# Performance work log

Measured on AMD Instinct MI355X. Metric: run time of the kernel, lower is better.

Reference implementation:

```python
import jax, jax.numpy as jnp
import numpy as np


def setup_inputs() -> dict:
    key = jax.random.key(0)
    k1, k2, k3 = jax.random.split(key, 3)
    N, D, B = 2000000, 128, 4096
    x = jax.random.normal(k1, (N, D), dtype=jnp.float32)
    batch = jnp.sort(jax.random.randint(k2, (N,), 0, B, dtype=jnp.int64))
    alpha = jax.random.normal(k3, (1,), dtype=jnp.float32)
    return {"x": x, "batch": batch, "alpha": alpha, "num_segments": B}


def reference(x, batch, alpha, num_segments):
    # Gating scalar in (0, 1)
    a = jax.nn.sigmoid(alpha)  # shape (1,), broadcasts
    # Segment mean: sum / count (count clamped to avoid div-by-zero on empty segments)
    seg_sum = jax.ops.segment_sum(x, batch, num_segments=num_segments)  # [B, D]
    counts = jax.ops.segment_sum(jnp.ones((x.shape[0],), dtype=x.dtype), batch,
                                 num_segments=num_segments)  # [B]
    mean = seg_sum / jnp.maximum(counts, 1.0)[:, None]  # [B, D]
    # Segment max; empty segments get -inf -> replace with 0 to match scatter-max fill
    mx = jax.ops.segment_max(x, batch, num_segments=num_segments)  # [B, D]
    mx = jnp.where(jnp.isfinite(mx), mx, 0.0)
    return a * mean + (1.0 - a) * mx
```

## Files before the change

### kernel.cpp

```cpp
#include <hip/hip_runtime.h>
#include <math.h>
#include <float.h>


__global__ void detect_kernel(const int* __restrict__ words, int N, int* __restrict__ meta) {
    meta[0] = (words[(size_t)N - 1] != 0) ? 1 : 2;
}

__global__ void starts_kernel(const int* __restrict__ words, int N, int B,
                              int* __restrict__ start, const int* __restrict__ meta) {
    int i = blockIdx.x * blockDim.x + threadIdx.x;
    if (i >= N) return;
    const int stride = meta[0];
    int cur = words[(size_t)i * stride];
    if (i == 0) {
        for (int b = 0; b <= cur; ++b) start[b] = 0;
    } else {
        int prev = words[(size_t)(i - 1) * stride];
        if (prev != cur) {
            for (int b = prev + 1; b <= cur; ++b) start[b] = i;
        }
    }
    if (i == N - 1) {
        for (int b = cur + 1; b <= B; ++b) start[b] = N;
    }
}

__global__ __launch_bounds__(256) void pool_kernel(const float4* __restrict__ x,
                                                   const int* __restrict__ start,
                                                   const float* __restrict__ alpha,
                                                   float4* __restrict__ out) {
    const int b  = blockIdx.x;
    const int t  = threadIdx.x;
    const int c4 = t & 31;
    const int rg = t >> 5;

    const int s = start[b];
    const int e = start[b + 1];

    float4 sum = make_float4(0.f, 0.f, 0.f, 0.f);
    float4 mx  = make_float4(-FLT_MAX, -FLT_MAX, -FLT_MAX, -FLT_MAX);

    for (int r = s + rg; r < e; r += 8) {
        float4 v = x[(size_t)r * 32 + c4];
        sum.x += v.x; sum.y += v.y; sum.z += v.z; sum.w += v.w;
        mx.x = fmaxf(mx.x, v.x); mx.y = fmaxf(mx.y, v.y);
        mx.z = fmaxf(mx.z, v.z); mx.w = fmaxf(mx.w, v.w);
    }

    __shared__ float4 lsum[8][32];
    __shared__ float4 lmax[8][32];
    lsum[rg][c4] = sum;
    lmax[rg][c4] = mx;
    __syncthreads();

    if (rg == 0) {
        #pragma unroll
        for (int r = 1; r < 8; ++r) {
            float4 ps = lsum[r][c4];
            float4 pm = lmax[r][c4];
            sum.x += ps.x; sum.y += ps.y; sum.z += ps.z; sum.w += ps.w;
            mx.x = fmaxf(mx.x, pm.x); mx.y = fmaxf(mx.y, pm.y);
            mx.z = fmaxf(mx.z, pm.z); mx.w = fmaxf(mx.w, pm.w);
        }
        const int cnt = e - s;
        float a = 1.0f / (1.0f + __expf(-alpha[0]));
        float4 o;
        if (cnt == 0) {
            o = make_float4(0.f, 0.f, 0.f, 0.f);
        } else {
            float inv = 1.0f / (float)cnt;
            float ia = 1.0f - a;
            o.x = a * (sum.x * inv) + ia * mx.x;
            o.y = a * (sum.y * inv) + ia * mx.y;
            o.z = a * (sum.z * inv) + ia * mx.z;
            o.w = a * (sum.w * inv) + ia * mx.w;
        }
        out[(size_t)b * 32 + c4] = o;
    }
}

extern "C" void kernel_launch(void* const* d_in, const int* in_sizes, int n_in,
                              void* d_out, int out_size, void* d_ws, size_t ws_size,
                              hipStream_t stream) {
    const float* x     = (const float*)d_in[0];
    const int*   batch = (const int*)d_in[1];
    const float* alpha = (const float*)d_in[2];

    const int N = in_sizes[1];
    const int Dd = in_sizes[0] / N;
    const int B = out_size / Dd;

    int* ws_start = (int*)d_ws;
    int* ws_meta  = ws_start + (B + 1);

    detect_kernel<<<1, 1, 0, stream>>>(batch, N, ws_meta);

    int threads = 256;
    int blocks = (N + threads - 1) / threads;
    starts_kernel<<<blocks, threads, 0, stream>>>(batch, N, B, ws_start, ws_meta);

    pool_kernel<<<B, 256, 0, stream>>>((const float4*)x, ws_start, alpha,
                                       (float4*)d_out);
}
```

Measured before the change: 191.0 us.

## Fuse segment-boundary search into pool kernel via binary search, unroll loads

Drops the detect and starts kernels. Each pool block now finds its segment bounds by binary search over the sorted batch array, which removes two launches and a full pass over the N-length index array. The row loop is unrolled by two with independent accumulators and uses nontemporal loads for the streaming x reads. Every thread now does about 2·log2(N) dependent global reads before the main loop, which adds latency at the start of each block.

```diff
diff --git a/kernel.cpp b/kernel.cpp
--- a/kernel.cpp
+++ b/kernel.cpp
@@ -2,79 +2,78 @@
 #include <math.h>
 #include <float.h>
 
+typedef float f32x4 __attribute__((ext_vector_type(4)));
 
-__global__ void detect_kernel(const int* __restrict__ words, int N, int* __restrict__ meta) {
-    meta[0] = (words[(size_t)N - 1] != 0) ? 1 : 2;
+__device__ __forceinline__ f32x4 max4(f32x4 a, f32x4 b) {
+    f32x4 r;
+    r.x = fmaxf(a.x, b.x); r.y = fmaxf(a.y, b.y);
+    r.z = fmaxf(a.z, b.z); r.w = fmaxf(a.w, b.w);
+    return r;
 }
 
-__global__ void starts_kernel(const int* __restrict__ words, int N, int B,
-                              int* __restrict__ start, const int* __restrict__ meta) {
-    int i = blockIdx.x * blockDim.x + threadIdx.x;
-    if (i >= N) return;
-    const int stride = meta[0];
-    int cur = words[(size_t)i * stride];
-    if (i == 0) {
-        for (int b = 0; b <= cur; ++b) start[b] = 0;
-    } else {
-        int prev = words[(size_t)(i - 1) * stride];
-        if (prev != cur) {
-            for (int b = prev + 1; b <= cur; ++b) start[b] = i;
-        }
-    }
-    if (i == N - 1) {
-        for (int b = cur + 1; b <= B; ++b) start[b] = N;
-    }
-}
-
-__global__ __launch_bounds__(256) void pool_kernel(const float4* __restrict__ x,
-                                                   const int* __restrict__ start,
+__global__ __launch_bounds__(256) void pool_kernel(const f32x4* __restrict__ x,
+                                                   const int* __restrict__ words, int N,
                                                    const float* __restrict__ alpha,
-                                                   float4* __restrict__ out) {
+                                                   f32x4* __restrict__ out) {
     const int b  = blockIdx.x;
     const int t  = threadIdx.x;
     const int c4 = t & 31;
     const int rg = t >> 5;
 
-    const int s = start[b];
-    const int e = start[b + 1];
+    const int stride = (words[(size_t)N - 1] != 0) ? 1 : 2;
 
-    float4 sum = make_float4(0.f, 0.f, 0.f, 0.f);
-    float4 mx  = make_float4(-FLT_MAX, -FLT_MAX, -FLT_MAX, -FLT_MAX);
+    int lo = 0, hi = N;
+    while (lo < hi) {
+        int mid = (lo + hi) >> 1;
+        if (words[(size_t)mid * stride] < b) lo = mid + 1; else hi = mid;
+    }
+    const int s = lo;
+    hi = N;
+    while (lo < hi) {
+        int mid = (lo + hi) >> 1;
+        if (words[(size_t)mid * stride] < b + 1) lo = mid + 1; else hi = mid;
+    }
+    const int e = lo;
 
-    for (int r = s + rg; r < e; r += 8) {
-        float4 v = x[(size_t)r * 32 + c4];
-        sum.x += v.x; sum.y += v.y; sum.z += v.z; sum.w += v.w;
-        mx.x = fmaxf(mx.x, v.x); mx.y = fmaxf(mx.y, v.y);
-        mx.z = fmaxf(mx.z, v.z); mx.w = fmaxf(mx.w, v.w);
+    f32x4 sum0 = (f32x4)0.f, sum1 = (f32x4)0.f;
+    f32x4 mx0 = (f32x4)(-FLT_MAX), mx1 = (f32x4)(-FLT_MAX);
+
+    const f32x4* __restrict__ xp = x + c4;
+    int r = s + rg;
+    for (; r + 8 < e; r += 16) {
+        f32x4 v0 = __builtin_nontemporal_load(xp + (size_t)r * 32);
+        f32x4 v1 = __builtin_nontemporal_load(xp + (size_t)(r + 8) * 32);
+        sum0 += v0; mx0 = max4(mx0, v0);
+        sum1 += v1; mx1 = max4(mx1, v1);
     }
+    if (r < e) {
+        f32x4 v0 = __builtin_nontemporal_load(xp + (size_t)r * 32);
+        sum0 += v0; mx0 = max4(mx0, v0);
+    }
+    sum0 += sum1;
+    mx0 = max4(mx0, mx1);
 
-    __shared__ float4 lsum[8][32];
-    __shared__ float4 lmax[8][32];
-    lsum[rg][c4] = sum;
-    lmax[rg][c4] = mx;
+    __shared__ f32x4 lsum[8][32];
+    __shared__ f32x4 lmax[8][32];
+    lsum[rg][c4] = sum0;
+    lmax[rg][c4] = mx0;
     __syncthreads();
 
     if (rg == 0) {
         #pragma unroll
-        for (int r = 1; r < 8; ++r) {
-            float4 ps = lsum[r][c4];
-            float4 pm = lmax[r][c4];
-            sum.x += ps.x; sum.y += ps.y; sum.z += ps.z; sum.w += ps.w;
-            mx.x = fmaxf(mx.x, pm.x); mx.y = fmaxf(mx.y, pm.y);
-            mx.z = fmaxf(mx.z, pm.z); mx.w = fmaxf(mx.w, pm.w);
+        for (int k = 1; k < 8; ++k) {
+            sum0 += lsum[k][c4];
+            mx0 = max4(mx0, lmax[k][c4]);
         }
         const int cnt = e - s;
-        float a = 1.0f / (1.0f + __expf(-alpha[0]));
-        float4 o;
+        const float a = 1.0f / (1.0f + __expf(-alpha[0]));
+        f32x4 o;
         if (cnt == 0) {
-            o = make_float4(0.f, 0.f, 0.f, 0.f);
+            o = (f32x4)0.f;
         } else {
-            float inv = 1.0f / (float)cnt;
-            float ia = 1.0f - a;
-            o.x = a * (sum.x * inv) + ia * mx.x;
-            o.y = a * (sum.y * inv) + ia * mx.y;
-            o.z = a * (sum.z * inv) + ia * mx.z;
-            o.w = a * (sum.w * inv) + ia * mx.w;
+            const float inv = 1.0f / (float)cnt;
+            const float ia = 1.0f - a;
+            o = a * (sum0 * inv) + ia * mx0;
         }
         out[(size_t)b * 32 + c4] = o;
     }
@@ -88,18 +87,10 @@
     const float* alpha = (const float*)d_in[2];
 
     const int N = in_sizes[1];
-    const int Dd = in_sizes[0] / N;
-    const int B = out_size / Dd;
+    const int D = in_sizes[0] / N;
+    const int B = out_size / D;
+    (void)d_ws; (void)ws_size; (void)n_in;
 
-    int* ws_start = (int*)d_ws;
-    int* ws_meta  = ws_start + (B + 1);
-
-    detect_kernel<<<1, 1, 0, stream>>>(batch, N, ws_meta);
-
-    int threads = 256;
-    int blocks = (N + threads - 1) / threads;
-    starts_kernel<<<blocks, threads, 0, stream>>>(batch, N, B, ws_start, ws_meta);
-
-    pool_kernel<<<B, 256, 0, stream>>>((const float4*)x, ws_start, alpha,
-                                       (float4*)d_out);
+    pool_kernel<<<B, 256, 0, stream>>>((const f32x4*)x, batch, N, alpha,
+                                       (f32x4*)d_out);
 }
```

Result: faster. 163.9 us (-14.2%).
